# Performance work log

Hardware: AMD Instinct MI355X
Metric: run time of the kernel (lower is better)

Reference implementation:

```python
import jax, jax.numpy as jnp
import numpy as np


def _rot_yx(angle):
    # [...,] -> [..., 2, 2] rotation matrix (yx convention)
    c, s = jnp.cos(angle), jnp.sin(angle)
    return jnp.stack([jnp.stack([c, -s], axis=-1),
                      jnp.stack([s, c], axis=-1)], axis=-2)


def setup_inputs() -> dict:
    key = jax.random.key(0)
    k1, k2 = jax.random.split(key)
    bboxes = jax.random.normal(k1, (4, 2048, 4, 2), dtype=jnp.float32)  # [B,N,4 corners,2 (y,x)]
    angles = jax.random.normal(k2, (4, 2048), dtype=jnp.float32)        # [B,N]
    return {"bboxes": bboxes, "angles": angles}


def reference(bboxes, angles):
    # --- bbox -> Gaussian (u, sigma) ---
    center = jnp.mean(bboxes, axis=-2, keepdims=True)                   # [B,N,1,2]
    pts = jnp.matmul(bboxes - center, _rot_yx(-angles))                 # de-rotated corners [B,N,4,2]
    size = jnp.max(pts, axis=-2) - jnp.min(pts, axis=-2)                # [B,N,2]
    R = _rot_yx(angles)                                                 # [B,N,2,2]
    delta = (size / 2)[..., :, None] * jnp.eye(2, dtype=bboxes.dtype)   # diag(size/2)
    sigma = jnp.einsum('bnij,bnjk,bnlk->bnil', R, delta, R)             # R @ delta @ R^T [B,N,2,2]
    u = center[..., 0, :]                                               # [B,N,2]

    # --- all-pairs Gaussian IoU (broadcast instead of repeat+transpose) ---
    u_diff = u[:, :, None, :] - u[:, None, :, :]                        # [B,N,N,2]
    s = (sigma[:, :, None] + sigma[:, None, :]) / 2                     # [B,N,N,2,2]
    a, b, c, d = s[..., 0, 0], s[..., 0, 1], s[..., 1, 0], s[..., 1, 1]
    det = a * d - b * c                                                 # [B,N,N]
    inv_det = jnp.where(det == 0, 0.0, 1.0 / jnp.where(det == 0, 1.0, det))  # divide_no_nan
    # original einsum '...id,...dd,...id' takes the DIAGONAL of inv_sigma: diag = [d, a] * inv_det
    inv_diag = jnp.stack([d, a], axis=-1) * inv_det[..., None]          # [B,N,N,2]
    Bd = jnp.sum((u_diff / 8) * inv_diag * u_diff, axis=-1)             # [B,N,N]
    det_s = sigma[..., 0, 0] * sigma[..., 1, 1] - sigma[..., 0, 1] * sigma[..., 1, 0]  # [B,N]
    Bd = Bd + 0.5 * jnp.log(det / jnp.sqrt(det_s[:, :, None] * det_s[:, None, :]))
    Bc = jnp.exp(-Bd)
    Hd = jnp.sqrt(jnp.maximum(1.0 - Bc, 1e-12))                         # eps-floor guards diag self-pairs
    return 1.0 - Hd
```

## Files before the change

kernel.cpp:

```cpp
#include <hip/hip_runtime.h>

constexpr int BATCH = 4;
constexpr int NBOX  = 2048;
constexpr int NB    = BATCH * NBOX;
constexpr int TPB   = 256;
constexpr int JQ    = 4;
constexpr int JSPAN = TPB * JQ;
constexpr int ITILE = 16;
constexpr float NL8E = -0.18033688011112042f;


__global__ __launch_bounds__(TPB) void precompute_params(
        const float* __restrict__ bboxes,
        const float* __restrict__ angles,
        float* __restrict__ P) {
    int idx = blockIdx.x * TPB + threadIdx.x;
    if (idx >= NB) return;

    const float4* bp = reinterpret_cast<const float4*>(bboxes) + (size_t)idx * 2;
    float4 p01 = bp[0];
    float4 p23 = bp[1];

    float cx = (p01.x + p01.z + p23.x + p23.z) * 0.25f;
    float cy = (p01.y + p01.w + p23.y + p23.w) * 0.25f;

    float ang = angles[idx];
    float s = __sinf(ang);
    float c = __cosf(ang);

    float dx0 = p01.x - cx, dy0 = p01.y - cy;
    float dx1 = p01.z - cx, dy1 = p01.w - cy;
    float dx2 = p23.x - cx, dy2 = p23.y - cy;
    float dx3 = p23.z - cx, dy3 = p23.w - cy;

    float px0 = dx0 * c - dy0 * s, py0 = dx0 * s + dy0 * c;
    float px1 = dx1 * c - dy1 * s, py1 = dx1 * s + dy1 * c;
    float px2 = dx2 * c - dy2 * s, py2 = dx2 * s + dy2 * c;
    float px3 = dx3 * c - dy3 * s, py3 = dx3 * s + dy3 * c;

    float minx = fminf(fminf(px0, px1), fminf(px2, px3));
    float maxx = fmaxf(fmaxf(px0, px1), fmaxf(px2, px3));
    float miny = fminf(fminf(py0, py1), fminf(py2, py3));
    float maxy = fmaxf(fmaxf(py0, py1), fmaxf(py2, py3));

    float w0 = (maxx - minx) * 0.5f;
    float w1 = (maxy - miny) * 0.5f;

    P[0 * NB + idx] = cx;
    P[1 * NB + idx] = cy;
    P[2 * NB + idx] = 0.5f * (c * c * w0 + s * s * w1);
    P[3 * NB + idx] = 0.5f * (c * s * (w0 - w1));
    P[4 * NB + idx] = 0.5f * (s * s * w0 + c * c * w1);
    P[5 * NB + idx] = __builtin_amdgcn_sqrtf(__builtin_amdgcn_sqrtf(w0 * w1));
}

__device__ __forceinline__ float pair_iou(
        float iux, float iuy, float ia, float ib, float id, float ir,
        float jux, float juy, float ja, float jb, float jd, float jr) {
    float ddx = iux - jux;
    float ddy = iuy - juy;
    float a   = ia + ja;
    float bb  = ib + jb;
    float d   = id + jd;
    float det = a * d - bb * bb;
    float rsq = __builtin_amdgcn_rsqf(det);
    float inv = rsq * rsq;
    float q   = (ddx * ddx) * d + (ddy * ddy) * a;
    float e   = (q * inv) * NL8E;
    float bc  = __builtin_amdgcn_exp2f(e) * (rsq * (ir * jr));
    float hd  = __builtin_amdgcn_sqrtf(fmaxf(1.0f - bc, 1e-12f));
    return 1.0f - hd;
}

__global__ __launch_bounds__(TPB) void pairwise_iou(
        const float* __restrict__ P,
        float* __restrict__ out) {
    const int tid = threadIdx.x;
    const int b   = blockIdx.z;
    const int i0  = blockIdx.y * ITILE;
    const int j0  = blockIdx.x * JSPAN + tid * JQ;

    __shared__ float sp[6][ITILE];
    if (tid < 6 * ITILE) {
        int f = tid >> 4;
        int k = tid & (ITILE - 1);
        sp[f][k] = P[f * NB + b * NBOX + i0 + k];
    }

    const int gj = b * NBOX + j0;
    float4 jux = *reinterpret_cast<const float4*>(P + 0 * NB + gj);
    float4 juy = *reinterpret_cast<const float4*>(P + 1 * NB + gj);
    float4 jA  = *reinterpret_cast<const float4*>(P + 2 * NB + gj);
    float4 jB  = *reinterpret_cast<const float4*>(P + 3 * NB + gj);
    float4 jD  = *reinterpret_cast<const float4*>(P + 4 * NB + gj);
    float4 jR  = *reinterpret_cast<const float4*>(P + 5 * NB + gj);
    __syncthreads();

    float* orow = out + ((size_t)(b * NBOX + i0)) * NBOX + j0;

    #pragma unroll 4
    for (int it = 0; it < ITILE; ++it) {
        float iux = sp[0][it];
        float iuy = sp[1][it];
        float ia  = sp[2][it];
        float ibv = sp[3][it];
        float id  = sp[4][it];
        float ir  = sp[5][it];

        float4 r;
        r.x = pair_iou(iux, iuy, ia, ibv, id, ir, jux.x, juy.x, jA.x, jB.x, jD.x, jR.x);
        r.y = pair_iou(iux, iuy, ia, ibv, id, ir, jux.y, juy.y, jA.y, jB.y, jD.y, jR.y);
        r.z = pair_iou(iux, iuy, ia, ibv, id, ir, jux.z, juy.z, jA.z, jB.z, jD.z, jR.z);
        r.w = pair_iou(iux, iuy, ia, ibv, id, ir, jux.w, juy.w, jA.w, jB.w, jD.w, jR.w);

        *reinterpret_cast<float4*>(orow + (size_t)it * NBOX) = r;
    }
}

extern "C" void kernel_launch(void* const* d_in, const int* in_sizes, int n_in,
                              void* d_out, int out_size, void* d_ws, size_t ws_size,
                              hipStream_t stream) {
    const float* bboxes = (const float*)d_in[0];
    const float* angles = (const float*)d_in[1];
    float* out = (float*)d_out;
    float* P   = (float*)d_ws;

    dim3 g1(NB / TPB);
    precompute_params<<<g1, TPB, 0, stream>>>(bboxes, angles, P);

    dim3 g2(NBOX / JSPAN, NBOX / ITILE, BATCH);
    pairwise_iou<<<g2, TPB, 0, stream>>>(P, out);
}
```

Baseline: 25.59 us.

## Fuse box parameter precompute into pairwise IoU kernel and pack math as float2

Drops the separate precompute kernel and its workspace round-trip. Each block now recomputes the Gaussian parameters for its 16 i-boxes and each thread for its 4 j-boxes, straight from bboxes and angles. The pair math is restructured into float2 lanes so the compiler can emit packed FP32 ops, and launch bounds gain a min-blocks hint. This removes one kernel launch and the dependency between kernels, at the cost of redundant trig and min/max work repeated across 128 i-tile blocks.

After: 24.10 us. 1.06x faster.

```diff
diff --git a/kernel.cpp b/kernel.cpp
--- a/kernel.cpp
+++ b/kernel.cpp
@@ -2,27 +2,20 @@
 
 constexpr int BATCH = 4;
 constexpr int NBOX  = 2048;
-constexpr int NB    = BATCH * NBOX;
 constexpr int TPB   = 256;
 constexpr int JQ    = 4;
 constexpr int JSPAN = TPB * JQ;
 constexpr int ITILE = 16;
 constexpr float NL8E = -0.18033688011112042f;
 
+__device__ __forceinline__ void box_params(
+        const float4* __restrict__ bb4, const float* __restrict__ angles, int idx,
+        float& cx, float& cy, float& A, float& B, float& D, float& R) {
+    float4 p01 = bb4[2 * idx];
+    float4 p23 = bb4[2 * idx + 1];
 
-__global__ __launch_bounds__(TPB) void precompute_params(
-        const float* __restrict__ bboxes,
-        const float* __restrict__ angles,
-        float* __restrict__ P) {
-    int idx = blockIdx.x * TPB + threadIdx.x;
-    if (idx >= NB) return;
-
-    const float4* bp = reinterpret_cast<const float4*>(bboxes) + (size_t)idx * 2;
-    float4 p01 = bp[0];
-    float4 p23 = bp[1];
-
-    float cx = (p01.x + p01.z + p23.x + p23.z) * 0.25f;
-    float cy = (p01.y + p01.w + p23.y + p23.w) * 0.25f;
+    cx = (p01.x + p01.z + p23.x + p23.z) * 0.25f;
+    cy = (p01.y + p01.w + p23.y + p23.w) * 0.25f;
 
     float ang = angles[idx];
     float s = __sinf(ang);
@@ -46,54 +39,78 @@
     float w0 = (maxx - minx) * 0.5f;
     float w1 = (maxy - miny) * 0.5f;
 
-    P[0 * NB + idx] = cx;
-    P[1 * NB + idx] = cy;
-    P[2 * NB + idx] = 0.5f * (c * c * w0 + s * s * w1);
-    P[3 * NB + idx] = 0.5f * (c * s * (w0 - w1));
-    P[4 * NB + idx] = 0.5f * (s * s * w0 + c * c * w1);
-    P[5 * NB + idx] = __builtin_amdgcn_sqrtf(__builtin_amdgcn_sqrtf(w0 * w1));
+    A = 0.5f * (c * c * w0 + s * s * w1);
+    B = 0.5f * (c * s * (w0 - w1));
+    D = 0.5f * (s * s * w0 + c * c * w1);
+    R = __builtin_amdgcn_sqrtf(__builtin_amdgcn_sqrtf(w0 * w1));
 }
 
-__device__ __forceinline__ float pair_iou(
-        float iux, float iuy, float ia, float ib, float id, float ir,
-        float jux, float juy, float ja, float jb, float jd, float jr) {
-    float ddx = iux - jux;
-    float ddy = iuy - juy;
-    float a   = ia + ja;
-    float bb  = ib + jb;
-    float d   = id + jd;
-    float det = a * d - bb * bb;
-    float rsq = __builtin_amdgcn_rsqf(det);
-    float inv = rsq * rsq;
-    float q   = (ddx * ddx) * d + (ddy * ddy) * a;
-    float e   = (q * inv) * NL8E;
-    float bc  = __builtin_amdgcn_exp2f(e) * (rsq * (ir * jr));
-    float hd  = __builtin_amdgcn_sqrtf(fmaxf(1.0f - bc, 1e-12f));
-    return 1.0f - hd;
+__device__ __forceinline__ float2 f2(float x, float y) { return make_float2(x, y); }
+__device__ __forceinline__ float2 add2(float2 a, float2 b) { return f2(a.x + b.x, a.y + b.y); }
+__device__ __forceinline__ float2 sub2(float2 a, float2 b) { return f2(a.x - b.x, a.y - b.y); }
+__device__ __forceinline__ float2 mul2(float2 a, float2 b) { return f2(a.x * b.x, a.y * b.y); }
+__device__ __forceinline__ float2 fma2(float2 a, float2 b, float2 c) {
+    return f2(__builtin_fmaf(a.x, b.x, c.x), __builtin_fmaf(a.y, b.y, c.y));
 }
 
-__global__ __launch_bounds__(TPB) void pairwise_iou(
-        const float* __restrict__ P,
+__device__ __forceinline__ float2 pair_duo(
+        float iux, float iuy, float ia, float ib, float id, float ir,
+        float2 jux, float2 juy, float2 ja, float2 jb, float2 jd, float2 jr) {
+    float2 ddx = sub2(f2(iux, iux), jux);
+    float2 ddy = sub2(f2(iuy, iuy), juy);
+    float2 a   = add2(f2(ia, ia), ja);
+    float2 bb  = add2(f2(ib, ib), jb);
+    float2 d   = add2(f2(id, id), jd);
+
+    float2 mb2 = mul2(bb, bb);
+    float2 det = fma2(a, d, f2(-mb2.x, -mb2.y));
+    float2 rsq = f2(__builtin_amdgcn_rsqf(det.x), __builtin_amdgcn_rsqf(det.y));
+    float2 inv = mul2(rsq, rsq);
+
+    float2 q   = fma2(mul2(ddy, ddy), a, mul2(mul2(ddx, ddx), d));
+    float2 e   = mul2(mul2(q, inv), f2(NL8E, NL8E));
+    float2 ex  = f2(__builtin_amdgcn_exp2f(e.x), __builtin_amdgcn_exp2f(e.y));
+
+    float2 bc  = mul2(mul2(ex, rsq), mul2(f2(ir, ir), jr));
+    float2 om  = f2(fmaxf(1.0f - bc.x, 1e-12f), fmaxf(1.0f - bc.y, 1e-12f));
+    float2 hd  = f2(__builtin_amdgcn_sqrtf(om.x), __builtin_amdgcn_sqrtf(om.y));
+    return f2(1.0f - hd.x, 1.0f - hd.y);
+}
+
+__global__ __launch_bounds__(TPB, 4) void fused_iou(
+        const float* __restrict__ bboxes,
+        const float* __restrict__ angles,
         float* __restrict__ out) {
     const int tid = threadIdx.x;
     const int b   = blockIdx.z;
     const int i0  = blockIdx.y * ITILE;
     const int j0  = blockIdx.x * JSPAN + tid * JQ;
 
+    const float4* bb4 = reinterpret_cast<const float4*>(bboxes);
+
     __shared__ float sp[6][ITILE];
-    if (tid < 6 * ITILE) {
-        int f = tid >> 4;
-        int k = tid & (ITILE - 1);
-        sp[f][k] = P[f * NB + b * NBOX + i0 + k];
+    if (tid < ITILE) {
+        float cx, cy, A, B, D, R;
+        box_params(bb4, angles, b * NBOX + i0 + tid, cx, cy, A, B, D, R);
+        sp[0][tid] = cx; sp[1][tid] = cy; sp[2][tid] = A;
+        sp[3][tid] = B;  sp[4][tid] = D;  sp[5][tid] = R;
     }
 
-    const int gj = b * NBOX + j0;
-    float4 jux = *reinterpret_cast<const float4*>(P + 0 * NB + gj);
-    float4 juy = *reinterpret_cast<const float4*>(P + 1 * NB + gj);
-    float4 jA  = *reinterpret_cast<const float4*>(P + 2 * NB + gj);
-    float4 jB  = *reinterpret_cast<const float4*>(P + 3 * NB + gj);
-    float4 jD  = *reinterpret_cast<const float4*>(P + 4 * NB + gj);
-    float4 jR  = *reinterpret_cast<const float4*>(P + 5 * NB + gj);
+    float jp[6][JQ];
+    #pragma unroll
+    for (int q = 0; q < JQ; ++q) {
+        float cx, cy, A, B, D, R;
+        box_params(bb4, angles, b * NBOX + j0 + q, cx, cy, A, B, D, R);
+        jp[0][q] = cx; jp[1][q] = cy; jp[2][q] = A;
+        jp[3][q] = B;  jp[4][q] = D;  jp[5][q] = R;
+    }
+    float2 jux0 = f2(jp[0][0], jp[0][1]), jux1 = f2(jp[0][2], jp[0][3]);
+    float2 juy0 = f2(jp[1][0], jp[1][1]), juy1 = f2(jp[1][2], jp[1][3]);
+    float2 jA0  = f2(jp[2][0], jp[2][1]), jA1  = f2(jp[2][2], jp[2][3]);
+    float2 jB0  = f2(jp[3][0], jp[3][1]), jB1  = f2(jp[3][2], jp[3][3]);
+    float2 jD0  = f2(jp[4][0], jp[4][1]), jD1  = f2(jp[4][2], jp[4][3]);
+    float2 jR0  = f2(jp[5][0], jp[5][1]), jR1  = f2(jp[5][2], jp[5][3]);
+
     __syncthreads();
 
     float* orow = out + ((size_t)(b * NBOX + i0)) * NBOX + j0;
@@ -107,13 +124,11 @@
         float id  = sp[4][it];
         float ir  = sp[5][it];
 
-        float4 r;
-        r.x = pair_iou(iux, iuy, ia, ibv, id, ir, jux.x, juy.x, jA.x, jB.x, jD.x, jR.x);
-        r.y = pair_iou(iux, iuy, ia, ibv, id, ir, jux.y, juy.y, jA.y, jB.y, jD.y, jR.y);
-        r.z = pair_iou(iux, iuy, ia, ibv, id, ir, jux.z, juy.z, jA.z, jB.z, jD.z, jR.z);
-        r.w = pair_iou(iux, iuy, ia, ibv, id, ir, jux.w, juy.w, jA.w, jB.w, jD.w, jR.w);
+        float2 r01 = pair_duo(iux, iuy, ia, ibv, id, ir, jux0, juy0, jA0, jB0, jD0, jR0);
+        float2 r23 = pair_duo(iux, iuy, ia, ibv, id, ir, jux1, juy1, jA1, jB1, jD1, jR1);
 
-        *reinterpret_cast<float4*>(orow + (size_t)it * NBOX) = r;
+        *reinterpret_cast<float4*>(orow) = make_float4(r01.x, r01.y, r23.x, r23.y);
+        orow += NBOX;
     }
 }
 
@@ -123,11 +138,7 @@
     const float* bboxes = (const float*)d_in[0];
     const float* angles = (const float*)d_in[1];
     float* out = (float*)d_out;
-    float* P   = (float*)d_ws;
 
-    dim3 g1(NB / TPB);
-    precompute_params<<<g1, TPB, 0, stream>>>(bboxes, angles, P);
-
-    dim3 g2(NBOX / JSPAN, NBOX / ITILE, BATCH);
-    pairwise_iou<<<g2, TPB, 0, stream>>>(P, out);
+    dim3 g(NBOX / JSPAN, NBOX / ITILE, BATCH);
+    fused_iou<<<g, TPB, 0, stream>>>(bboxes, angles, out);
 }
```

## Retile pairwise kernel to full-row blocks with packed float2 math and nontemporal stores

Applied to the files above, without the earlier changes.

Each block now handles 4 full i-rows across all 2048 j columns, where it previously covered a 16-row by 1024-column tile. The i-parameters are held in registers instead of shared memory, which removes the __syncthreads. The pair computation is written with float2 helpers so the compiler can emit packed FP32 ops. Output is written with nontemporal stores to avoid polluting the cache. The trade-off is more j-parameter reloads per output and a different grid shape, so the kernel may stay bound by output write bandwidth.

Result: no change. 25.13 us (-1.8%).

```diff
diff --git a/kernel.cpp b/kernel.cpp
--- a/kernel.cpp
+++ b/kernel.cpp
@@ -5,10 +5,12 @@
 constexpr int NB    = BATCH * NBOX;
 constexpr int TPB   = 256;
 constexpr int JQ    = 4;
-constexpr int JSPAN = TPB * JQ;
-constexpr int ITILE = 16;
+constexpr int JCHUNK = TPB * JQ;
+constexpr int NCHUNK = NBOX / JCHUNK;
+constexpr int IROWS = 4;
 constexpr float NL8E = -0.18033688011112042f;
 
+typedef float f32x4 __attribute__((ext_vector_type(4)));
 
 __global__ __launch_bounds__(TPB) void precompute_params(
         const float* __restrict__ bboxes,
@@ -54,66 +56,87 @@
     P[5 * NB + idx] = __builtin_amdgcn_sqrtf(__builtin_amdgcn_sqrtf(w0 * w1));
 }
 
-__device__ __forceinline__ float pair_iou(
-        float iux, float iuy, float ia, float ib, float id, float ir,
-        float jux, float juy, float ja, float jb, float jd, float jr) {
-    float ddx = iux - jux;
-    float ddy = iuy - juy;
-    float a   = ia + ja;
-    float bb  = ib + jb;
-    float d   = id + jd;
-    float det = a * d - bb * bb;
-    float rsq = __builtin_amdgcn_rsqf(det);
-    float inv = rsq * rsq;
-    float q   = (ddx * ddx) * d + (ddy * ddy) * a;
-    float e   = (q * inv) * NL8E;
-    float bc  = __builtin_amdgcn_exp2f(e) * (rsq * (ir * jr));
-    float hd  = __builtin_amdgcn_sqrtf(fmaxf(1.0f - bc, 1e-12f));
-    return 1.0f - hd;
+__device__ __forceinline__ float2 f2(float x, float y) { return make_float2(x, y); }
+__device__ __forceinline__ float2 add2(float2 a, float2 b) { return f2(a.x + b.x, a.y + b.y); }
+__device__ __forceinline__ float2 sub2(float2 a, float2 b) { return f2(a.x - b.x, a.y - b.y); }
+__device__ __forceinline__ float2 mul2(float2 a, float2 b) { return f2(a.x * b.x, a.y * b.y); }
+__device__ __forceinline__ float2 fma2(float2 a, float2 b, float2 c) {
+    return f2(__builtin_fmaf(a.x, b.x, c.x), __builtin_fmaf(a.y, b.y, c.y));
 }
 
-__global__ __launch_bounds__(TPB) void pairwise_iou(
+__device__ __forceinline__ float2 pair_duo(
+        float iux, float iuy, float ia, float ib, float id, float ir,
+        float2 jux, float2 juy, float2 ja, float2 jb, float2 jd, float2 jr) {
+    float2 ddx = sub2(f2(iux, iux), jux);
+    float2 ddy = sub2(f2(iuy, iuy), juy);
+    float2 a   = add2(f2(ia, ia), ja);
+    float2 bb  = add2(f2(ib, ib), jb);
+    float2 d   = add2(f2(id, id), jd);
+
+    float2 mb2 = mul2(bb, bb);
+    float2 det = fma2(a, d, f2(-mb2.x, -mb2.y));
+    float2 rsq = f2(__builtin_amdgcn_rsqf(det.x), __builtin_amdgcn_rsqf(det.y));
+    float2 inv = mul2(rsq, rsq);
+
+    float2 q   = fma2(mul2(ddy, ddy), a, mul2(mul2(ddx, ddx), d));
+    float2 e   = mul2(mul2(q, inv), f2(NL8E, NL8E));
+    float2 ex  = f2(__builtin_amdgcn_exp2f(e.x), __builtin_amdgcn_exp2f(e.y));
+
+    float2 bc  = mul2(mul2(ex, rsq), mul2(f2(ir, ir), jr));
+    float2 om  = f2(fmaxf(1.0f - bc.x, 1e-12f), fmaxf(1.0f - bc.y, 1e-12f));
+    float2 hd  = f2(__builtin_amdgcn_sqrtf(om.x), __builtin_amdgcn_sqrtf(om.y));
+    return f2(1.0f - hd.x, 1.0f - hd.y);
+}
+
+__global__ __launch_bounds__(TPB, 8) void pairwise_rows(
         const float* __restrict__ P,
         float* __restrict__ out) {
     const int tid = threadIdx.x;
-    const int b   = blockIdx.z;
-    const int i0  = blockIdx.y * ITILE;
-    const int j0  = blockIdx.x * JSPAN + tid * JQ;
+    const int b   = blockIdx.y;
+    const int i0  = blockIdx.x * IROWS;
+    const int gi  = b * NBOX + i0;
 
-    __shared__ float sp[6][ITILE];
-    if (tid < 6 * ITILE) {
-        int f = tid >> 4;
-        int k = tid & (ITILE - 1);
-        sp[f][k] = P[f * NB + b * NBOX + i0 + k];
+    float iux[IROWS], iuy[IROWS], iA[IROWS], iB[IROWS], iD[IROWS], iR[IROWS];
+    #pragma unroll
+    for (int r = 0; r < IROWS; ++r) {
+        iux[r] = P[0 * NB + gi + r];
+        iuy[r] = P[1 * NB + gi + r];
+        iA[r]  = P[2 * NB + gi + r];
+        iB[r]  = P[3 * NB + gi + r];
+        iD[r]  = P[4 * NB + gi + r];
+        iR[r]  = P[5 * NB + gi + r];
     }
 
-    const int gj = b * NBOX + j0;
-    float4 jux = *reinterpret_cast<const float4*>(P + 0 * NB + gj);
-    float4 juy = *reinterpret_cast<const float4*>(P + 1 * NB + gj);
-    float4 jA  = *reinterpret_cast<const float4*>(P + 2 * NB + gj);
-    float4 jB  = *reinterpret_cast<const float4*>(P + 3 * NB + gj);
-    float4 jD  = *reinterpret_cast<const float4*>(P + 4 * NB + gj);
-    float4 jR  = *reinterpret_cast<const float4*>(P + 5 * NB + gj);
-    __syncthreads();
+    #pragma unroll
+    for (int jc = 0; jc < NCHUNK; ++jc) {
+        const int j0 = jc * JCHUNK + tid * JQ;
+        const int gj = b * NBOX + j0;
 
-    float* orow = out + ((size_t)(b * NBOX + i0)) * NBOX + j0;
+        float4 jux = *reinterpret_cast<const float4*>(P + 0 * NB + gj);
+        float4 juy = *reinterpret_cast<const float4*>(P + 1 * NB + gj);
+        float4 jA  = *reinterpret_cast<const float4*>(P + 2 * NB + gj);
+        float4 jB  = *reinterpret_cast<const float4*>(P + 3 * NB + gj);
+        float4 jD  = *reinterpret_cast<const float4*>(P + 4 * NB + gj);
+        float4 jR  = *reinterpret_cast<const float4*>(P + 5 * NB + gj);
 
-    #pragma unroll 4
-    for (int it = 0; it < ITILE; ++it) {
-        float iux = sp[0][it];
-        float iuy = sp[1][it];
-        float ia  = sp[2][it];
-        float ibv = sp[3][it];
-        float id  = sp[4][it];
-        float ir  = sp[5][it];
+        float2 jux01 = f2(jux.x, jux.y), jux23 = f2(jux.z, jux.w);
+        float2 juy01 = f2(juy.x, juy.y), juy23 = f2(juy.z, juy.w);
+        float2 jA01  = f2(jA.x, jA.y),   jA23  = f2(jA.z, jA.w);
+        float2 jB01  = f2(jB.x, jB.y),   jB23  = f2(jB.z, jB.w);
+        float2 jD01  = f2(jD.x, jD.y),   jD23  = f2(jD.z, jD.w);
+        float2 jR01  = f2(jR.x, jR.y),   jR23  = f2(jR.z, jR.w);
 
-        float4 r;
-        r.x = pair_iou(iux, iuy, ia, ibv, id, ir, jux.x, juy.x, jA.x, jB.x, jD.x, jR.x);
-        r.y = pair_iou(iux, iuy, ia, ibv, id, ir, jux.y, juy.y, jA.y, jB.y, jD.y, jR.y);
-        r.z = pair_iou(iux, iuy, ia, ibv, id, ir, jux.z, juy.z, jA.z, jB.z, jD.z, jR.z);
-        r.w = pair_iou(iux, iuy, ia, ibv, id, ir, jux.w, juy.w, jA.w, jB.w, jD.w, jR.w);
-
-        *reinterpret_cast<float4*>(orow + (size_t)it * NBOX) = r;
+        #pragma unroll
+        for (int r = 0; r < IROWS; ++r) {
+            float2 rlo = pair_duo(iux[r], iuy[r], iA[r], iB[r], iD[r], iR[r],
+                                  jux01, juy01, jA01, jB01, jD01, jR01);
+            float2 rhi = pair_duo(iux[r], iuy[r], iA[r], iB[r], iD[r], iR[r],
+                                  jux23, juy23, jA23, jB23, jD23, jR23);
+            f32x4 rv;
+            rv.x = rlo.x; rv.y = rlo.y; rv.z = rhi.x; rv.w = rhi.y;
+            __builtin_nontemporal_store(
+                rv, reinterpret_cast<f32x4*>(out + (size_t)(gi + r) * NBOX + j0));
+        }
     }
 }
 
@@ -125,9 +148,8 @@
     float* out = (float*)d_out;
     float* P   = (float*)d_ws;
 
-    dim3 g1(NB / TPB);
-    precompute_params<<<g1, TPB, 0, stream>>>(bboxes, angles, P);
+    precompute_params<<<dim3(NB / TPB), TPB, 0, stream>>>(bboxes, angles, P);
 
-    dim3 g2(NBOX / JSPAN, NBOX / ITILE, BATCH);
-    pairwise_iou<<<g2, TPB, 0, stream>>>(P, out);
+    dim3 g(NBOX / IROWS, BATCH);
+    pairwise_rows<<<g, TPB, 0, stream>>>(P, out);
 }
```
